# Performance work log

Hardware: AMD Instinct MI355X
Metric: run time of the kernel (lower is better)

Reference implementation:

```python
import jax, jax.numpy as jnp
import numpy as np

B = 2; C = 3; IMG = 224; P = 16
DIM = 256; DEPTH = 2; HEADS = 4; DH = 64; MLP = 1024; NCLS = 1000
GRID = IMG // P            # 14
NPATCH = GRID * GRID       # 196
T = NPATCH + 1             # 197 (cls token)
PATCH_DIM = C * P * P      # 768


def _ln(x, g, b):
    m = x.mean(-1, keepdims=True)
    v = ((x - m) ** 2).mean(-1, keepdims=True)
    return (x - m) * jax.lax.rsqrt(v + 1e-5) * g + b


def _trittention(x, ln_g, ln_b, w_abcde, b_abcde, w_out, b_out):
    b, t, _ = x.shape
    xn = _ln(x, ln_g, ln_b)
    abcde = xn @ w_abcde + b_abcde                      # [b,t,5*H*DH]
    a, bb, c, d, e = jnp.split(abcde, 5, axis=-1)
    rs = lambda z: z.reshape(b, t, HEADS, DH)
    a, bb, c, d, e = map(rs, (a, bb, c, d, e))
    # cubic ternary scores: [b, h, q, s, t]
    s = jnp.einsum('bshd,bthd,bqhd->bhqst', a, bb, c) / DH
    p = jax.nn.softmax(s.reshape(b, HEADS, t, t * t), axis=-1)
    p = p.reshape(b, HEADS, t, t, t)
    z = jnp.einsum('bhqlr,blhd->bhqd', p, d) + jnp.einsum('bhqlr,brhd->bhqd', p, e)
    z = z.transpose(0, 2, 1, 3).reshape(b, t, HEADS * DH)
    return z @ w_out + b_out


def _ff(x, ln_g, ln_b, w1, b1, w2, b2):
    h = jax.nn.gelu(_ln(x, ln_g, ln_b) @ w1 + b1, approximate=False)
    return h @ w2 + b2


def setup_inputs() -> dict:
    key = jax.random.key(0)
    ks = jax.random.split(key, 10)
    s = 0.02
    d = {}
    d['img'] = jax.random.normal(ks[0], (B, C, IMG, IMG), jnp.float32)
    d['patch_ln1_g'] = jnp.ones((PATCH_DIM,), jnp.float32)
    d['patch_ln1_b'] = jnp.zeros((PATCH_DIM,), jnp.float32)
    d['patch_w'] = jax.random.normal(ks[1], (PATCH_DIM, DIM), jnp.float32) * s
    d['patch_b'] = jnp.zeros((DIM,), jnp.float32)
    d['patch_ln2_g'] = jnp.ones((DIM,), jnp.float32)
    d['patch_ln2_b'] = jnp.zeros((DIM,), jnp.float32)
    d['pos_emb'] = jax.random.normal(ks[2], (1, T, DIM), jnp.float32) * s
    d['cls_token'] = jax.random.normal(ks[3], (1, 1, DIM), jnp.float32) * s
    d['attn_ln_g'] = jnp.ones((DEPTH, DIM), jnp.float32)
    d['attn_ln_b'] = jnp.zeros((DEPTH, DIM), jnp.float32)
    d['w_abcde'] = jax.random.normal(ks[4], (DEPTH, DIM, 5 * HEADS * DH), jnp.float32) * s
    d['b_abcde'] = jnp.zeros((DEPTH, 5 * HEADS * DH), jnp.float32)
    d['w_out'] = jax.random.normal(ks[5], (DEPTH, HEADS * DH, DIM), jnp.float32) * s
    d['b_out'] = jnp.zeros((DEPTH, DIM), jnp.float32)
    d['ff_ln_g'] = jnp.ones((DEPTH, DIM), jnp.float32)
    d['ff_ln_b'] = jnp.zeros((DEPTH, DIM), jnp.float32)
    d['ff_w1'] = jax.random.normal(ks[6], (DEPTH, DIM, MLP), jnp.float32) * s
    d['ff_b1'] = jnp.zeros((DEPTH, MLP), jnp.float32)
    d['ff_w2'] = jax.random.normal(ks[7], (DEPTH, MLP, DIM), jnp.float32) * s
    d['ff_b2'] = jnp.zeros((DEPTH, DIM), jnp.float32)
    d['final_ln_g'] = jnp.ones((DIM,), jnp.float32)
    d['final_ln_b'] = jnp.zeros((DIM,), jnp.float32)
    d['head_w'] = jax.random.normal(ks[8], (DIM, NCLS), jnp.float32) * s
    d['head_b'] = jnp.zeros((NCLS,), jnp.float32)
    return d


def reference(img, patch_ln1_g, patch_ln1_b, patch_w, patch_b, patch_ln2_g, patch_ln2_b,
              pos_emb, cls_token, attn_ln_g, attn_ln_b, w_abcde, b_abcde, w_out, b_out,
              ff_ln_g, ff_ln_b, ff_w1, ff_b1, ff_w2, ff_b2, final_ln_g, final_ln_b,
              head_w, head_b):
    b = img.shape[0]
    # Rearrange 'b c (h p1) (w p2) -> b (h w) (p1 p2 c)'
    x = img.reshape(b, C, GRID, P, GRID, P).transpose(0, 2, 4, 3, 5, 1)
    x = x.reshape(b, NPATCH, PATCH_DIM)
    x = _ln(x, patch_ln1_g, patch_ln1_b)
    x = x @ patch_w + patch_b
    x = _ln(x, patch_ln2_g, patch_ln2_b)
    cls = jnp.broadcast_to(cls_token, (b, 1, DIM))
    x = jnp.concatenate([cls, x], axis=1) + pos_emb
    for i in range(DEPTH):
        x = _trittention(x, attn_ln_g[i], attn_ln_b[i], w_abcde[i], b_abcde[i],
                         w_out[i], b_out[i]) + x
        x = _ff(x, ff_ln_g[i], ff_ln_b[i], ff_w1[i], ff_b1[i], ff_w2[i], ff_b2[i]) + x
    x = _ln(x, final_ln_g, final_ln_b)
    return x[:, 0] @ head_w + head_b
```

## Files before the change

kernel.cpp:

```cpp
#include <hip/hip_runtime.h>
#include <hip/hip_bf16.h>

#define BB 2
#define TT 197
#define TP 208
#define NT16 13
#define DIMM 256
#define HEADS_ 4
#define DH_ 64
#define ABCDE_N 1280
#define MLP_ 1024
#define NCLS_ 1000
#define PATCH_DIM_ 768

typedef __attribute__((ext_vector_type(8))) short short8_t;
typedef __attribute__((ext_vector_type(4))) float f32x4;

__device__ __forceinline__ float waveReduceSum(float v) {
#pragma unroll
    for (int off = 32; off > 0; off >>= 1) v += __shfl_xor(v, off, 64);
    return v;
}

__device__ __forceinline__ float rowReduceSum16(float v) {
    v += __uint_as_float(__builtin_amdgcn_update_dpp(
            0, __float_as_uint(v), 0x121, 0xF, 0xF, true));
    v += __uint_as_float(__builtin_amdgcn_update_dpp(
            0, __float_as_uint(v), 0x122, 0xF, 0xF, true));
    v += __uint_as_float(__builtin_amdgcn_update_dpp(
            0, __float_as_uint(v), 0x124, 0xF, 0xF, true));
    v += __uint_as_float(__builtin_amdgcn_update_dpp(
            0, __float_as_uint(v), 0x128, 0xF, 0xF, true));
    return v;
}

__device__ __forceinline__ unsigned short f2bf(float x) {
    unsigned int u = __float_as_uint(x);
    u += 0x7FFFu + ((u >> 16) & 1u);
    return (unsigned short)(u >> 16);
}

__device__ __forceinline__ float bf2f(unsigned short u) {
    return __uint_as_float(((unsigned int)u) << 16);
}

__global__ __launch_bounds__(1024) void patch_embed_k(
    const float* __restrict__ img, const float* __restrict__ g1, const float* __restrict__ b1,
    const float* __restrict__ pw, const float* __restrict__ pb,
    const float* __restrict__ g2, const float* __restrict__ b2,
    const float* __restrict__ pos, const float* __restrict__ cls,
    float* __restrict__ xa)
{
    int tid = threadIdx.x;
    if (blockIdx.x == 98) {
        if (tid < DIMM)
            for (int b = 0; b < BB; b++)
                xa[(long)b * TT * DIMM + tid] = cls[tid] + pos[tid];
        return;
    }
    __shared__ __align__(16) float xs[4][PATCH_DIM_];
    __shared__ float psum[4][4][DIMM];
    __shared__ float red[8];
    int pr0 = blockIdx.x * 4;
    int wv16 = tid >> 6, lane = tid & 63;

    for (int i = tid; i < 4 * PATCH_DIM_; i += 1024) {
        int r = i / PATCH_DIM_, j = i - r * PATCH_DIM_;
        int pr = pr0 + r;
        int b = pr / 196, patch = pr % 196;
        int gh = patch / 14, gw = patch % 14;
        int c = j % 3, p2 = (j / 3) % 16, p1 = j / 48;
        xs[r][j] = img[(((long)b * 3 + c) * 224 + gh * 16 + p1) * 224 + gw * 16 + p2];
    }
    __syncthreads();
    if (wv16 < 4) {
        int r = wv16;
        float s = 0.f, s2 = 0.f;
        for (int j = lane; j < PATCH_DIM_; j += 64) { float v = xs[r][j]; s += v; s2 += v * v; }
        s = waveReduceSum(s); s2 = waveReduceSum(s2);
        float m = s / PATCH_DIM_;
        float rs = rsqrtf(s2 / PATCH_DIM_ - m * m + 1e-5f);
        for (int j = lane; j < PATCH_DIM_; j += 64)
            xs[r][j] = (xs[r][j] - m) * rs * g1[j] + b1[j];
    }
    __syncthreads();
    int col = tid & 255, ks = tid >> 8;
    int k0 = ks * (PATCH_DIM_ / 4);
    float acc[4] = {0.f, 0.f, 0.f, 0.f};
    for (int k = k0; k < k0 + PATCH_DIM_ / 4; k += 4) {
        float w0 = pw[(k + 0) * DIMM + col];
        float w1 = pw[(k + 1) * DIMM + col];
        float w2 = pw[(k + 2) * DIMM + col];
        float w3 = pw[(k + 3) * DIMM + col];
#pragma unroll
        for (int r = 0; r < 4; r++) {
            float4 xv = *(const float4*)&xs[r][k];
            acc[r] = fmaf(xv.x, w0, fmaf(xv.y, w1, fmaf(xv.z, w2, fmaf(xv.w, w3, acc[r]))));
        }
    }
#pragma unroll
    for (int r = 0; r < 4; r++) psum[ks][r][col] = acc[r];
    __syncthreads();

    float v4[4];
    if (tid < 256) {
#pragma unroll
        for (int r = 0; r < 4; r++)
            v4[r] = (psum[0][r][tid] + psum[1][r][tid])
                  + (psum[2][r][tid] + psum[3][r][tid]) + pb[tid];
    }
    for (int r = 0; r < 4; r++) {
        float s = 0.f, s2 = 0.f;
        if (tid < 256) {
            s = waveReduceSum(v4[r]);
            s2 = waveReduceSum(v4[r] * v4[r]);
            if (lane == 0) { red[wv16 * 2] = s; red[wv16 * 2 + 1] = s2; }
        }
        __syncthreads();
        float S = red[0] + red[2] + red[4] + red[6];
        float S2 = red[1] + red[3] + red[5] + red[7];
        __syncthreads();
        if (tid < 256) {
            float m = S / DIMM;
            float rs = rsqrtf(S2 / DIMM - m * m + 1e-5f);
            int pr = pr0 + r;
            int b = pr / 196, patch = pr % 196;
            float v = (v4[r] - m) * rs * g2[tid] + b2[tid] + pos[(1 + patch) * DIMM + tid];
            xa[((long)b * TT + 1 + patch) * DIMM + tid] = v;
        }
    }
}

__global__ __launch_bounds__(512) void gemm_ksplit_k(
    const float* __restrict__ x, long x_stride, int M, int K, int N,
    const float* __restrict__ w, const float* __restrict__ bias,
    const float* __restrict__ res, float* __restrict__ out,
    const float* __restrict__ ln_g, const float* __restrict__ ln_b,
    int do_gelu)
{
    __shared__ __align__(16) float xs[4 * 1024];
    __shared__ float psum[8 * 4 * 64];
    int tid = threadIdx.x, lane = tid & 63, wv = tid >> 6;
    int row0 = blockIdx.y * 4, col0 = blockIdx.x * 64;

    for (int i = tid; i < 4 * K; i += 512) {
        int r = i / K, k = i - r * K;
        int row = row0 + r;
        xs[i] = (row < M) ? x[(long)row * x_stride + k] : 0.f;
    }
    __syncthreads();
    if (ln_g) {
        if (wv < 4) {
            float* xr = xs + wv * K;
            float s = 0.f, s2 = 0.f;
            for (int k = lane; k < K; k += 64) { float v = xr[k]; s += v; s2 += v * v; }
            s = waveReduceSum(s); s2 = waveReduceSum(s2);
            float m = s / K;
            float rs = rsqrtf(s2 / K - m * m + 1e-5f);
            for (int k = lane; k < K; k += 64)
                xr[k] = (xr[k] - m) * rs * ln_g[k] + ln_b[k];
        }
        __syncthreads();
    }

    int col = col0 + lane;
    float a0 = 0.f, a1 = 0.f, a2 = 0.f, a3 = 0.f;
    int kq = K >> 3;
    if (col < N) {
        const float* x0 = xs + wv * kq;
        const float* x1 = x0 + K;
        const float* x2 = x1 + K;
        const float* x3 = x2 + K;
        const float* wp = w + (long)(wv * kq) * N + col;
        long nl = N;
        for (int kk = 0; kk < kq; kk += 4) {
            float w0 = wp[0], w1 = wp[nl], w2 = wp[2 * nl], w3 = wp[3 * nl];
            wp += 4 * nl;
            float4 v0 = *(const float4*)(x0 + kk);
            float4 v1 = *(const float4*)(x1 + kk);
            float4 v2 = *(const float4*)(x2 + kk);
            float4 v3 = *(const float4*)(x3 + kk);
            a0 = fmaf(v0.x, w0, fmaf(v0.y, w1, fmaf(v0.z, w2, fmaf(v0.w, w3, a0))));
            a1 = fmaf(v1.x, w0, fmaf(v1.y, w1, fmaf(v1.z, w2, fmaf(v1.w, w3, a1))));
            a2 = fmaf(v2.x, w0, fmaf(v2.y, w1, fmaf(v2.z, w2, fmaf(v2.w, w3, a2))));
            a3 = fmaf(v3.x, w0, fmaf(v3.y, w1, fmaf(v3.z, w2, fmaf(v3.w, w3, a3))));
        }
    }
    psum[wv * 256 + 0 * 64 + lane] = a0;
    psum[wv * 256 + 1 * 64 + lane] = a1;
    psum[wv * 256 + 2 * 64 + lane] = a2;
    psum[wv * 256 + 3 * 64 + lane] = a3;
    __syncthreads();

    if (tid < 256) {
        int r = tid >> 6, c = tid & 63;
        float v = ((psum[r * 64 + c]        + psum[256 + r * 64 + c])
                +  (psum[512 + r * 64 + c]  + psum[768 + r * 64 + c]))
                + ((psum[1024 + r * 64 + c] + psum[1280 + r * 64 + c])
                +  (psum[1536 + r * 64 + c] + psum[1792 + r * 64 + c]));
        int row = row0 + r, cw = col0 + c;
        if (row < M && cw < N) {
            if (bias) v += bias[cw];
            if (do_gelu) v = 0.5f * v * (1.f + erff(v * 0.70710678118654752f));
            if (res) v += res[(long)row * N + cw];
            out[(long)row * N + cw] = v;
        }
    }
}

__global__ __launch_bounds__(512) void gemm_ksplit4_k(
    const float* __restrict__ x, long x_stride, int M, int K, int N,
    const float* __restrict__ w, const float* __restrict__ bias,
    const float* __restrict__ res, float* __restrict__ out,
    const float* __restrict__ ln_g, const float* __restrict__ ln_b,
    int do_gelu)
{
    __shared__ __align__(16) float xs[4 * 1024];
    __shared__ float psum[8 * 4 * 256];
    int tid = threadIdx.x, lane = tid & 63, wv = tid >> 6;
    int row0 = blockIdx.y * 4, col0 = blockIdx.x * 256;

    for (int i = tid; i < 4 * K; i += 512) {
        int r = i / K, k = i - r * K;
        int row = row0 + r;
        xs[i] = (row < M) ? x[(long)row * x_stride + k] : 0.f;
    }
    __syncthreads();
    if (ln_g) {
        if (wv < 4) {
            float* xr = xs + wv * K;
            float s = 0.f, s2 = 0.f;
            for (int k = lane; k < K; k += 64) { float v = xr[k]; s += v; s2 += v * v; }
            s = waveReduceSum(s); s2 = waveReduceSum(s2);
            float m = s / K;
            float rs = rsqrtf(s2 / K - m * m + 1e-5f);
            for (int k = lane; k < K; k += 64)
                xr[k] = (xr[k] - m) * rs * ln_g[k] + ln_b[k];
        }
        __syncthreads();
    }

    int kq = K >> 3;
    float acc[4][4];
#pragma unroll
    for (int r = 0; r < 4; r++)
#pragma unroll
        for (int c = 0; c < 4; c++) acc[r][c] = 0.f;
    {
        const float* x0 = xs + wv * kq;
        const float* x1 = x0 + K;
        const float* x2 = x1 + K;
        const float* x3 = x2 + K;
        const float* wp = w + (long)(wv * kq) * N + col0 + lane;
        long nl = N;
        for (int kk = 0; kk < kq; kk += 2) {
            float wk0[4], wk1[4];
#pragma unroll
            for (int c = 0; c < 4; c++) {
                wk0[c] = wp[c * 64];
                wk1[c] = wp[nl + c * 64];
            }
            wp += 2 * nl;
            float2 v0 = *(const float2*)(x0 + kk);
            float2 v1 = *(const float2*)(x1 + kk);
            float2 v2 = *(const float2*)(x2 + kk);
            float2 v3 = *(const float2*)(x3 + kk);
#pragma unroll
            for (int c = 0; c < 4; c++) {
                acc[0][c] = fmaf(v0.x, wk0[c], fmaf(v0.y, wk1[c], acc[0][c]));
                acc[1][c] = fmaf(v1.x, wk0[c], fmaf(v1.y, wk1[c], acc[1][c]));
                acc[2][c] = fmaf(v2.x, wk0[c], fmaf(v2.y, wk1[c], acc[2][c]));
                acc[3][c] = fmaf(v3.x, wk0[c], fmaf(v3.y, wk1[c], acc[3][c]));
            }
        }
    }
#pragma unroll
    for (int r = 0; r < 4; r++)
#pragma unroll
        for (int c = 0; c < 4; c++)
            psum[wv * 1024 + r * 256 + c * 64 + lane] = acc[r][c];
    __syncthreads();

    for (int idx = tid; idx < 1024; idx += 512) {
        int r = idx >> 8, c = idx & 255;
        float v = ((psum[r * 256 + c]        + psum[1024 + r * 256 + c])
                +  (psum[2048 + r * 256 + c] + psum[3072 + r * 256 + c]))
                + ((psum[4096 + r * 256 + c] + psum[5120 + r * 256 + c])
                +  (psum[6144 + r * 256 + c] + psum[7168 + r * 256 + c]));
        int row = row0 + r, cw = col0 + c;
        if (row < M && cw < N) {
            if (bias) v += bias[cw];
            if (do_gelu) v = 0.5f * v * (1.f + erff(v * 0.70710678118654752f));
            if (res) v += res[(long)row * N + cw];
            out[(long)row * N + cw] = v;
        }
    }
}

__global__ __launch_bounds__(256) void tritt_k(
    const float* __restrict__ abcde, float* __restrict__ z)
{
    __shared__ __align__(16) unsigned short a_lds[TP * 64];
    __shared__ __align__(16) unsigned short b_lds[TP * 64];
    __shared__ float pl_s[4][TP];
    __shared__ float pr_s[4][TP];

    int tid = threadIdx.x, lane = tid & 63, wv = tid >> 6;
    int bh = blockIdx.y;
    int b = bh >> 2, h = bh & 3;
    const float* base = abcde + (long)b * TT * ABCDE_N;
    const float SC = 1.4426950408889634f / 64.f;

    for (int i = tid; i < TP * 8; i += 256) {
        int row = i >> 3, ch = i & 7;
        int idx = row * 64 + ((ch * 8) ^ ((row & 7) << 3));
        unsigned short av[8], bv[8];
        if (row < TT) {
            const float* srcA = base + (long)row * ABCDE_N + h * 64 + ch * 8;
            const float* srcB = srcA + 256;
            float4 a0 = *(const float4*)(srcA);
            float4 a1 = *(const float4*)(srcA + 4);
            float4 b0 = *(const float4*)(srcB);
            float4 b1 = *(const float4*)(srcB + 4);
            av[0] = f2bf(a0.x); av[1] = f2bf(a0.y); av[2] = f2bf(a0.z); av[3] = f2bf(a0.w);
            av[4] = f2bf(a1.x); av[5] = f2bf(a1.y); av[6] = f2bf(a1.z); av[7] = f2bf(a1.w);
            bv[0] = f2bf(b0.x); bv[1] = f2bf(b0.y); bv[2] = f2bf(b0.z); bv[3] = f2bf(b0.w);
            bv[4] = f2bf(b1.x); bv[5] = f2bf(b1.y); bv[6] = f2bf(b1.z); bv[7] = f2bf(b1.w);
        } else {
#pragma unroll
            for (int j = 0; j < 8; j++) { av[j] = 0; bv[j] = 0; }
        }
        *(short8_t*)&a_lds[idx] = *(const short8_t*)av;
        *(short8_t*)&b_lds[idx] = *(const short8_t*)bv;
    }
    __syncthreads();

    int q = blockIdx.x * 4 + wv;
    if (q >= TT) return;

    int lm = lane & 15;
    int lg = lane >> 4;

    const float* cp = base + (long)q * ABCDE_N + 512 + h * 64;
    float c0[8], c1[8];
    {
        float4 v0 = *(const float4*)(cp + lg * 8);
        float4 v1 = *(const float4*)(cp + lg * 8 + 4);
        float4 v2 = *(const float4*)(cp + (lg + 4) * 8);
        float4 v3 = *(const float4*)(cp + (lg + 4) * 8 + 4);
        c0[0] = v0.x * SC; c0[1] = v0.y * SC; c0[2] = v0.z * SC; c0[3] = v0.w * SC;
        c0[4] = v1.x * SC; c0[5] = v1.y * SC; c0[6] = v1.z * SC; c0[7] = v1.w * SC;
        c1[0] = v2.x * SC; c1[1] = v2.y * SC; c1[2] = v2.z * SC; c1[3] = v2.w * SC;
        c1[4] = v3.x * SC; c1[5] = v3.y * SC; c1[6] = v3.z * SC; c1[7] = v3.w * SC;
    }

    short8_t bf0[NT16], bf1[NT16];
#pragma unroll
    for (int j = 0; j < NT16; j++) {
        int brow = j * 16 + lm;
        bf0[j] = *(const short8_t*)&b_lds[brow * 64 + (((lg    ) * 8) ^ ((brow & 7) << 3))];
        bf1[j] = *(const short8_t*)&b_lds[brow * 64 + (((lg + 4) * 8) ^ ((brow & 7) << 3))];
    }

    float pcol[NT16];
#pragma unroll
    for (int j = 0; j < NT16; j++) pcol[j] = 0.f;

    int arow = lm;
    short8_t af0 = *(const short8_t*)&a_lds[arow * 64 + (((lg    ) * 8) ^ ((arow & 7) << 3))];
    short8_t af1 = *(const short8_t*)&a_lds[arow * 64 + (((lg + 4) * 8) ^ ((arow & 7) << 3))];

#pragma unroll 1
    for (int i = 0; i < NT16; i++) {
        short8_t nf0 = af0, nf1 = af1;
        if (i + 1 < NT16) {
            int nrow = (i + 1) * 16 + lm;
            nf0 = *(const short8_t*)&a_lds[nrow * 64 + (((lg    ) * 8) ^ ((nrow & 7) << 3))];
            nf1 = *(const short8_t*)&a_lds[nrow * 64 + (((lg + 4) * 8) ^ ((nrow & 7) << 3))];
        }
        short8_t ac0, ac1;
#pragma unroll
        for (int e = 0; e < 8; e++) {
            ac0[e] = (short)f2bf(bf2f((unsigned short)af0[e]) * c0[e]);
            ac1[e] = (short)f2bf(bf2f((unsigned short)af1[e]) * c1[e]);
        }
        float prow[4] = {0.f, 0.f, 0.f, 0.f};
#pragma unroll
        for (int j = 0; j < NT16; j++) {
            f32x4 acc = {0.f, 0.f, 0.f, 0.f};
            acc = __builtin_amdgcn_mfma_f32_16x16x32_bf16(ac0, bf0[j], acc, 0, 0, 0);
            acc = __builtin_amdgcn_mfma_f32_16x16x32_bf16(ac1, bf1[j], acc, 0, 0, 0);
            float e0 = __builtin_amdgcn_exp2f(acc[0]);
            float e1 = __builtin_amdgcn_exp2f(acc[1]);
            float e2 = __builtin_amdgcn_exp2f(acc[2]);
            float e3 = __builtin_amdgcn_exp2f(acc[3]);
            prow[0] += e0; prow[1] += e1; prow[2] += e2; prow[3] += e3;
            pcol[j] += (e0 + e1) + (e2 + e3);
        }
#pragma unroll
        for (int r = 0; r < 4; r++) prow[r] = rowReduceSum16(prow[r]);
        if (lm == 0) {
            int rb = i * 16 + lg * 4;
#pragma unroll
            for (int r = 0; r < 4; r++) pl_s[wv][rb + r] = prow[r];
        }
        af0 = nf0; af1 = nf1;
    }
#pragma unroll
    for (int j = 0; j < NT16; j++) {
        float c = pcol[j];
        c += __shfl_xor(c, 16, 64);
        c += __shfl_xor(c, 32, 64);
        if (lane < 16) pr_s[wv][j * 16 + lane] = c;
    }

    float zpart = 0.f;
    for (int s = lane; s < TT; s += 64) zpart += pl_s[wv][s];
    zpart = waveReduceSum(zpart);
    float rz = 1.f / (zpart - 11.f * TT);

    const float* dp = base + 768 + h * 64 + lane;
    const float* ep = base + 1024 + h * 64 + lane;
    float z0 = 0.f, z1 = 0.f, z2 = 0.f, z3 = 0.f;
    int s = 0;
    for (; s + 1 < TT; s += 2) {
        z0 = fmaf(pl_s[wv][s]     - 11.f, dp[(long)s * ABCDE_N],       z0);
        z1 = fmaf(pr_s[wv][s]     - 11.f, ep[(long)s * ABCDE_N],       z1);
        z2 = fmaf(pl_s[wv][s + 1] - 11.f, dp[(long)(s + 1) * ABCDE_N], z2);
        z3 = fmaf(pr_s[wv][s + 1] - 11.f, ep[(long)(s + 1) * ABCDE_N], z3);
    }
    z0 = fmaf(pl_s[wv][s] - 11.f, dp[(long)s * ABCDE_N], z0);
    z1 = fmaf(pr_s[wv][s] - 11.f, ep[(long)s * ABCDE_N], z1);
    z[((long)b * TT + q) * DIMM + h * 64 + lane] = ((z0 + z1) + (z2 + z3)) * rz;
}

extern "C" void kernel_launch(void* const* d_in, const int* in_sizes, int n_in,
                              void* d_out, int out_size, void* d_ws, size_t ws_size,
                              hipStream_t stream)
{
    const float* img    = (const float*)d_in[0];
    const float* g1     = (const float*)d_in[1];
    const float* b1     = (const float*)d_in[2];
    const float* pw     = (const float*)d_in[3];
    const float* pb     = (const float*)d_in[4];
    const float* g2     = (const float*)d_in[5];
    const float* b2     = (const float*)d_in[6];
    const float* pos    = (const float*)d_in[7];
    const float* cls    = (const float*)d_in[8];
    const float* attn_g = (const float*)d_in[9];
    const float* attn_b = (const float*)d_in[10];
    const float* w_abc  = (const float*)d_in[11];
    const float* b_abc  = (const float*)d_in[12];
    const float* w_out  = (const float*)d_in[13];
    const float* b_out  = (const float*)d_in[14];
    const float* ff_g   = (const float*)d_in[15];
    const float* ff_b   = (const float*)d_in[16];
    const float* w1     = (const float*)d_in[17];
    const float* b1f    = (const float*)d_in[18];
    const float* w2     = (const float*)d_in[19];
    const float* b2f    = (const float*)d_in[20];
    const float* fin_g  = (const float*)d_in[21];
    const float* fin_b  = (const float*)d_in[22];
    const float* hw     = (const float*)d_in[23];
    const float* hb     = (const float*)d_in[24];
    float* out = (float*)d_out;

    const int MROWS = BB * TT;
    float* ws = (float*)d_ws;
    float* xa = ws;
    float* xb = xa + (long)MROWS * DIMM;
    float* zb = xb + (long)MROWS * DIMM;
    float* ab = zb + (long)MROWS * DIMM;

    patch_embed_k<<<99, 1024, 0, stream>>>(img, g1, b1, pw, pb, g2, b2, pos, cls, xa);

    const int GY = (MROWS + 3) / 4;
    const int QT4 = (TT + 3) / 4;
    for (int i = 0; i < 2; i++) {
        gemm_ksplit4_k<<<dim3(ABCDE_N / 256, GY), 512, 0, stream>>>(
            xa, DIMM, MROWS, DIMM, ABCDE_N,
            w_abc + (long)i * DIMM * ABCDE_N, b_abc + (long)i * ABCDE_N,
            nullptr, ab, attn_g + i * DIMM, attn_b + i * DIMM, 0);
        tritt_k<<<dim3(QT4, BB * HEADS_), 256, 0, stream>>>(ab, zb);
        gemm_ksplit_k<<<dim3(DIMM / 64, GY), 512, 0, stream>>>(
            zb, DIMM, MROWS, DIMM, DIMM,
            w_out + (long)i * DIMM * DIMM, b_out + (long)i * DIMM,
            xa, xb, nullptr, nullptr, 0);
        gemm_ksplit4_k<<<dim3(MLP_ / 256, GY), 512, 0, stream>>>(
            xb, DIMM, MROWS, DIMM, MLP_,
            w1 + (long)i * DIMM * MLP_, b1f + (long)i * MLP_,
            nullptr, ab, ff_g + i * DIMM, ff_b + i * DIMM, 1);
        gemm_ksplit_k<<<dim3(DIMM / 64, GY), 512, 0, stream>>>(
            ab, MLP_, MROWS, MLP_, DIMM,
            w2 + (long)i * MLP_ * DIMM, b2f + (long)i * DIMM,
            xb, xa, nullptr, nullptr, 0);
    }
    gemm_ksplit_k<<<dim3((NCLS_ + 63) / 64, 1), 512, 0, stream>>>(
        xa, (long)TT * DIMM, BB, DIMM, NCLS_,
        hw, hb, nullptr, out, fin_g, fin_b, 0);
}
```

Before: 195.9 us.

## Split trittention score loop over two row halves with separate epilogue kernel

The trittention kernel is split into a main kernel that uses a z-dimension of 2 to divide the s-tile loop (7 and 6 tiles) across twice as many blocks. Row sums go to global memory directly, and partial column sums go to two global buffers. A new epilogue kernel adds the column partials, normalizes and computes the weighted d/e sums. The aim is to double the grid (400 to 800 blocks) for better CU occupancy, at the cost of an extra launch, global round-trips for the partial sums, and a duplicated B-tile load per block.

```diff
diff --git a/kernel.cpp b/kernel.cpp
--- a/kernel.cpp
+++ b/kernel.cpp
@@ -12,6 +12,7 @@
 #define MLP_ 1024
 #define NCLS_ 1000
 #define PATCH_DIM_ 768
+#define QPAD 200
 
 typedef __attribute__((ext_vector_type(8))) short short8_t;
 typedef __attribute__((ext_vector_type(4))) float f32x4;
@@ -297,41 +298,53 @@
     }
 }
 
-__global__ __launch_bounds__(256) void tritt_k(
-    const float* __restrict__ abcde, float* __restrict__ z)
+__global__ __launch_bounds__(256) void tritt_main_k(
+    const float* __restrict__ abcde, float* __restrict__ pl_g, float* __restrict__ pr_g)
 {
-    __shared__ __align__(16) unsigned short a_lds[TP * 64];
+    __shared__ __align__(16) unsigned short a_lds[112 * 64];
     __shared__ __align__(16) unsigned short b_lds[TP * 64];
-    __shared__ float pl_s[4][TP];
-    __shared__ float pr_s[4][TP];
 
     int tid = threadIdx.x, lane = tid & 63, wv = tid >> 6;
-    int bh = blockIdx.y;
+    int bh = blockIdx.y, z = blockIdx.z;
     int b = bh >> 2, h = bh & 3;
     const float* base = abcde + (long)b * TT * ABCDE_N;
     const float SC = 1.4426950408889634f / 64.f;
+    int i0 = z ? 7 : 0;
+    int nt = z ? 6 : 7;
+    int row0 = i0 * 16;
 
     for (int i = tid; i < TP * 8; i += 256) {
         int row = i >> 3, ch = i & 7;
         int idx = row * 64 + ((ch * 8) ^ ((row & 7) << 3));
-        unsigned short av[8], bv[8];
+        unsigned short bv[8];
         if (row < TT) {
-            const float* srcA = base + (long)row * ABCDE_N + h * 64 + ch * 8;
-            const float* srcB = srcA + 256;
-            float4 a0 = *(const float4*)(srcA);
-            float4 a1 = *(const float4*)(srcA + 4);
+            const float* srcB = base + (long)row * ABCDE_N + 256 + h * 64 + ch * 8;
             float4 b0 = *(const float4*)(srcB);
             float4 b1 = *(const float4*)(srcB + 4);
-            av[0] = f2bf(a0.x); av[1] = f2bf(a0.y); av[2] = f2bf(a0.z); av[3] = f2bf(a0.w);
-            av[4] = f2bf(a1.x); av[5] = f2bf(a1.y); av[6] = f2bf(a1.z); av[7] = f2bf(a1.w);
             bv[0] = f2bf(b0.x); bv[1] = f2bf(b0.y); bv[2] = f2bf(b0.z); bv[3] = f2bf(b0.w);
             bv[4] = f2bf(b1.x); bv[5] = f2bf(b1.y); bv[6] = f2bf(b1.z); bv[7] = f2bf(b1.w);
         } else {
 #pragma unroll
-            for (int j = 0; j < 8; j++) { av[j] = 0; bv[j] = 0; }
+            for (int j = 0; j < 8; j++) bv[j] = 0;
+        }
+        *(short8_t*)&b_lds[idx] = *(const short8_t*)bv;
+    }
+    for (int i = tid; i < nt * 16 * 8; i += 256) {
+        int rowl = i >> 3, ch = i & 7;
+        int row = row0 + rowl;
+        int idx = rowl * 64 + ((ch * 8) ^ ((rowl & 7) << 3));
+        unsigned short av[8];
+        if (row < TT) {
+            const float* srcA = base + (long)row * ABCDE_N + h * 64 + ch * 8;
+            float4 a0 = *(const float4*)(srcA);
+            float4 a1 = *(const float4*)(srcA + 4);
+            av[0] = f2bf(a0.x); av[1] = f2bf(a0.y); av[2] = f2bf(a0.z); av[3] = f2bf(a0.w);
+            av[4] = f2bf(a1.x); av[5] = f2bf(a1.y); av[6] = f2bf(a1.z); av[7] = f2bf(a1.w);
+        } else {
+#pragma unroll
+            for (int j = 0; j < 8; j++) av[j] = 0;
         }
         *(short8_t*)&a_lds[idx] = *(const short8_t*)av;
-        *(short8_t*)&b_lds[idx] = *(const short8_t*)bv;
     }
     __syncthreads();
 
@@ -366,15 +379,17 @@
 #pragma unroll
     for (int j = 0; j < NT16; j++) pcol[j] = 0.f;
 
+    float* plq = pl_g + ((long)bh * QPAD + q) * TP;
+
     int arow = lm;
     short8_t af0 = *(const short8_t*)&a_lds[arow * 64 + (((lg    ) * 8) ^ ((arow & 7) << 3))];
     short8_t af1 = *(const short8_t*)&a_lds[arow * 64 + (((lg + 4) * 8) ^ ((arow & 7) << 3))];
 
 #pragma unroll 1
-    for (int i = 0; i < NT16; i++) {
+    for (int il = 0; il < nt; il++) {
         short8_t nf0 = af0, nf1 = af1;
-        if (i + 1 < NT16) {
-            int nrow = (i + 1) * 16 + lm;
+        if (il + 1 < nt) {
+            int nrow = (il + 1) * 16 + lm;
             nf0 = *(const short8_t*)&a_lds[nrow * 64 + (((lg    ) * 8) ^ ((nrow & 7) << 3))];
             nf1 = *(const short8_t*)&a_lds[nrow * 64 + (((lg + 4) * 8) ^ ((nrow & 7) << 3))];
         }
@@ -400,18 +415,42 @@
 #pragma unroll
         for (int r = 0; r < 4; r++) prow[r] = rowReduceSum16(prow[r]);
         if (lm == 0) {
-            int rb = i * 16 + lg * 4;
-#pragma unroll
-            for (int r = 0; r < 4; r++) pl_s[wv][rb + r] = prow[r];
+            int rb = row0 + il * 16 + lg * 4;
+#pragma unroll
+            for (int r = 0; r < 4; r++) plq[rb + r] = prow[r];
         }
         af0 = nf0; af1 = nf1;
     }
+    float* prq = pr_g + (((long)z * 8 + bh) * QPAD + q) * TP;
 #pragma unroll
     for (int j = 0; j < NT16; j++) {
         float c = pcol[j];
         c += __shfl_xor(c, 16, 64);
         c += __shfl_xor(c, 32, 64);
-        if (lane < 16) pr_s[wv][j * 16 + lane] = c;
+        if (lane < 16) prq[j * 16 + lane] = c;
+    }
+}
+
+__global__ __launch_bounds__(256) void tritt_epi_k(
+    const float* __restrict__ abcde, const float* __restrict__ pl_g,
+    const float* __restrict__ pr_g, float* __restrict__ zout)
+{
+    __shared__ float pl_s[4][TP];
+    __shared__ float pr_s[4][TP];
+
+    int tid = threadIdx.x, lane = tid & 63, wv = tid >> 6;
+    int bh = blockIdx.y;
+    int b = bh >> 2, h = bh & 3;
+    const float* base = abcde + (long)b * TT * ABCDE_N;
+    int q = blockIdx.x * 4 + wv;
+    if (q >= TT) return;
+
+    const float* plq = pl_g + ((long)bh * QPAD + q) * TP;
+    const float* pr0 = pr_g + ((long)bh * QPAD + q) * TP;
+    const float* pr1 = pr_g + (((long)8 + bh) * QPAD + q) * TP;
+    for (int s = lane; s < TP; s += 64) {
+        pl_s[wv][s] = plq[s];
+        pr_s[wv][s] = pr0[s] + pr1[s];
     }
 
     float zpart = 0.f;
@@ -431,7 +470,7 @@
     }
     z0 = fmaf(pl_s[wv][s] - 11.f, dp[(long)s * ABCDE_N], z0);
     z1 = fmaf(pr_s[wv][s] - 11.f, ep[(long)s * ABCDE_N], z1);
-    z[((long)b * TT + q) * DIMM + h * 64 + lane] = ((z0 + z1) + (z2 + z3)) * rz;
+    zout[((long)b * TT + q) * DIMM + h * 64 + lane] = ((z0 + z1) + (z2 + z3)) * rz;
 }
 
 extern "C" void kernel_launch(void* const* d_in, const int* in_sizes, int n_in,
@@ -471,6 +510,8 @@
     float* xb = xa + (long)MROWS * DIMM;
     float* zb = xb + (long)MROWS * DIMM;
     float* ab = zb + (long)MROWS * DIMM;
+    float* pl = ab + (long)MROWS * ABCDE_N;
+    float* pr = pl + (long)8 * QPAD * TP;
 
     patch_embed_k<<<99, 1024, 0, stream>>>(img, g1, b1, pw, pb, g2, b2, pos, cls, xa);
 
@@ -481,7 +522,8 @@
             xa, DIMM, MROWS, DIMM, ABCDE_N,
             w_abc + (long)i * DIMM * ABCDE_N, b_abc + (long)i * ABCDE_N,
             nullptr, ab, attn_g + i * DIMM, attn_b + i * DIMM, 0);
-        tritt_k<<<dim3(QT4, BB * HEADS_), 256, 0, stream>>>(ab, zb);
+        tritt_main_k<<<dim3(QT4, BB * HEADS_, 2), 256, 0, stream>>>(ab, pl, pr);
+        tritt_epi_k<<<dim3(QT4, BB * HEADS_), 256, 0, stream>>>(ab, pl, pr, zb);
         gemm_ksplit_k<<<dim3(DIMM / 64, GY), 512, 0, stream>>>(
             zb, DIMM, MROWS, DIMM, DIMM,
             w_out + (long)i * DIMM * DIMM, b_out + (long)i * DIMM,
```

New measurement: 205.8 us. 1.05x slower.
